# Optimization experiments

Measured on AMD Instinct MI355X. Metric: run time of the kernel, lower is better.

## Reference

```python
import jax, jax.numpy as jnp
import numpy as np
from jax import lax

LMBD = 0.1      # l1 penalty weight (init kwarg lmbd)
TOL = 1e-4      # convergence tolerance (init kwarg tol)
N_ITERS = 1000  # max ISTA iterations
DICT_SIZE = 1024
INPUT_DIM = 512
BATCH = 256


def setup_inputs() -> dict:
    key = jax.random.key(0)
    kx, kd = jax.random.split(key)
    # Dictionary parameter: randn rows normalized to unit l2 norm (as in _init_dict)
    D = jax.random.normal(kd, (DICT_SIZE, INPUT_DIM), dtype=jnp.float32)
    D = D / jnp.linalg.norm(D, axis=1, keepdims=True)
    x = jax.random.normal(kx, (BATCH, INPUT_DIM), dtype=jnp.float32)
    return {"x": x, "D": D}


def reference(x, D):
    # lr = 0.99 / max eigenvalue of Gram(D)  (as in _init_lr, done under no_grad)
    gram = D @ D.T  # [dict, dict]
    lr = 0.99 / jnp.max(jnp.linalg.eigvalsh(gram))
    thresh = lr * LMBD
    h0 = jnp.zeros((x.shape[0], D.shape[0]), dtype=x.dtype)  # [batch, dict]

    def cond(state):
        _, i, delta = state
        return (i < N_ITERS) & (delta >= TOL)

    def body(state):
        h, i, _ = state
        resid = x - h @ D          # [batch, input_dim]
        g = resid @ D.T            # [batch, dict]
        a = h + lr * g
        h_new = jnp.sign(a) * jnp.maximum(jnp.abs(a) - thresh, 0.0)  # soft-threshold
        delta = jnp.max(jnp.linalg.norm(h_new - h, axis=1))
        return (h_new, i + 1, delta)

    h, _, _ = lax.while_loop(cond, body, (h0, jnp.int32(0), jnp.float32(jnp.inf)))
    return h
```

## Files before the change

kernel.cpp:

```cpp
#include <hip/hip_runtime.h>
#include <math.h>

#define DICT 1024
#define IN_DIM 512
#define BATCH 256
#define LMBD_F 0.1f
#define TOL2 1e-8f
#define MAX_ITERS 1000
#define LM 64

#define OFF_G      0u
#define OFF_B      1048576u
#define OFF_HA     1310720u
#define OFF_W      1572864u
#define OFF_RDP    1573888u
#define OFF_FLG    1577984u
#define OFF_PM     1582080u
#define OFF_BF     1582592u
#define OFF_GBF    2106880u

typedef __attribute__((ext_vector_type(8))) short short8v;
typedef __attribute__((ext_vector_type(4))) float f32x4;
typedef __attribute__((ext_vector_type(4))) int i32x4;

#define MFMA16(a, b, c) __builtin_amdgcn_mfma_f32_16x16x32_bf16(a, b, c, 0, 0, 0)

__device__ __forceinline__ ushort f2bf(float v) {
    union { float f; unsigned u; } x; x.f = v;
    unsigned r = x.u + 0x7fffu + ((x.u >> 16) & 1u);
    return (ushort)(r >> 16);
}
__device__ __forceinline__ float bf2f(ushort b) {
    union { unsigned u; float f; } x; x.u = ((unsigned)b) << 16;
    return x.f;
}
__device__ __forceinline__ float softthr(float aa, float th) {
    float s = fabsf(aa) - th;
    return s > 0.f ? copysignf(s, aa) : 0.f;
}

__device__ __forceinline__ void vmdrain() { asm volatile("s_waitcnt vmcnt(0)" ::: "memory"); }
__device__ __forceinline__ unsigned ld_flag(const unsigned* p) {
    unsigned v;
    asm volatile("global_load_dword %0, %1, off sc1\ns_waitcnt vmcnt(0)" : "=v"(v) : "v"(p) : "memory");
    return v;
}
__device__ __forceinline__ void st_flag(unsigned* p, unsigned v) {
    asm volatile("global_store_dword %0, %1, off sc1" :: "v"(p), "v"(v) : "memory");
}
__device__ __forceinline__ float ld_f_sc(const float* p) {
    float v;
    asm volatile("global_load_dword %0, %1, off sc1\ns_waitcnt vmcnt(0)" : "=v"(v) : "v"(p) : "memory");
    return v;
}
__device__ __forceinline__ void st_f_sc(float* p, float v) {
    asm volatile("global_store_dword %0, %1, off sc1" :: "v"(p), "v"(v) : "memory");
}
__device__ __forceinline__ f32x4 ld_f4_sc(const float* p) {
    f32x4 v;
    asm volatile("global_load_dwordx4 %0, %1, off sc1\ns_waitcnt vmcnt(0)" : "=v"(v) : "v"(p) : "memory");
    return v;
}
__device__ __forceinline__ void st_u_sc(unsigned* p, unsigned v) {
    asm volatile("global_store_dword %0, %1, off sc1" :: "v"(p), "v"(v) : "memory");
}
__device__ __forceinline__ void ld_a16(i32x4* d, const void* p) {
    asm volatile("global_load_dwordx4 %0, %1, off sc1" : "=v"(*d) : "v"(p));
}
__device__ __forceinline__ void ld_u_nw(unsigned* d, const unsigned* p) {
    asm volatile("global_load_dword %0, %1, off sc1" : "=v"(*d) : "v"(p));
}
__device__ __forceinline__ void ld_f_nw(float* d, const float* p) {
    asm volatile("global_load_dword %0, %1, off sc1" : "=v"(*d) : "v"(p));
}

__global__ void k_init(float* ws) {
    int t = threadIdx.x;
    unsigned* flg = (unsigned*)(ws + OFF_FLG);
#pragma unroll
    for (int j = 0; j < 4; ++j) flg[t + 1024 * j] = 0u;
#pragma unroll
    for (int j = 0; j < 4; ++j) ws[OFF_RDP + t + 1024 * j] = 1e30f;
    if (t == 0) *(unsigned*)(ws + OFF_PM) = 0u;
}

__global__ void k_gemm_nt(float* __restrict__ C, const float* __restrict__ A,
                          const float* __restrict__ B, int M, int N, int K) {
    __shared__ float As[32][33];
    __shared__ float Bs[32][33];
    const int tid = threadIdx.x;
    const int m0 = blockIdx.y * 32, n0 = blockIdx.x * 32;
    const int lrw = tid >> 3;
    const int lc4 = (tid & 7) * 4;
    const int ty = tid >> 4, tx = tid & 15;
    float acc00 = 0, acc01 = 0, acc10 = 0, acc11 = 0;
    for (int k0 = 0; k0 < K; k0 += 32) {
        float4 av = *(const float4*)&A[(m0 + lrw) * K + k0 + lc4];
        float4 bv = *(const float4*)&B[(n0 + lrw) * K + k0 + lc4];
        __syncthreads();
        As[lrw][lc4 + 0] = av.x; As[lrw][lc4 + 1] = av.y;
        As[lrw][lc4 + 2] = av.z; As[lrw][lc4 + 3] = av.w;
        Bs[lrw][lc4 + 0] = bv.x; Bs[lrw][lc4 + 1] = bv.y;
        Bs[lrw][lc4 + 2] = bv.z; Bs[lrw][lc4 + 3] = bv.w;
        __syncthreads();
#pragma unroll
        for (int k = 0; k < 32; ++k) {
            float a0 = As[ty * 2][k], a1 = As[ty * 2 + 1][k];
            float b0 = Bs[tx * 2][k], b1 = Bs[tx * 2 + 1][k];
            acc00 += a0 * b0; acc01 += a0 * b1;
            acc10 += a1 * b0; acc11 += a1 * b1;
        }
    }
    C[(m0 + ty * 2) * N + n0 + tx * 2] = acc00;
    C[(m0 + ty * 2) * N + n0 + tx * 2 + 1] = acc01;
    C[(m0 + ty * 2 + 1) * N + n0 + tx * 2] = acc10;
    C[(m0 + ty * 2 + 1) * N + n0 + tx * 2 + 1] = acc11;
}

__global__ void k_conv_g(float* ws) {
    const int i = (blockIdx.x * 256 + threadIdx.x) * 4;
    const float* G = ws + OFF_G;
    ushort* Ghi = (ushort*)(ws + OFF_GBF);
    ushort* Glo = Ghi + 1048576u;
    float4 g = *(const float4*)&G[i];
    ushort h0 = f2bf(g.x), h1 = f2bf(g.y), h2 = f2bf(g.z), h3 = f2bf(g.w);
    *(ushort4*)&Ghi[i] = make_ushort4(h0, h1, h2, h3);
    ushort l0 = f2bf(g.x - bf2f(h0)), l1 = f2bf(g.y - bf2f(h1));
    ushort l2 = f2bf(g.z - bf2f(h2)), l3 = f2bf(g.w - bf2f(h3));
    *(ushort4*)&Glo[i] = make_ushort4(l0, l1, l2, l3);
}

__launch_bounds__(512, 2)
__global__ void k_persist(float* __restrict__ ws, float* __restrict__ dout) {
    const int tid = threadIdx.x;
    const int bid = blockIdx.x;
    const int w = tid >> 6, lane = tid & 63;
    unsigned* flg = (unsigned*)(ws + OFF_FLG);
    unsigned* podmask = (unsigned*)(ws + OFF_PM);
    float* Wg = ws + OFF_W;
    float* rdp = ws + OFF_RDP;
    const float* G = ws + OFF_G;

    __shared__ float Ps[8][16][64];
    __shared__ float Vl[1024], VPl[1024], Wl[1024];
    __shared__ float aArr[LM], bArr[LM];
    __shared__ float sred[8];
    __shared__ float scal2[2];
    __shared__ unsigned sres;
    __shared__ unsigned sbits[16];
    __shared__ unsigned sStick;

    unsigned gen = 0;

    const int bx = bid & 15;
    const int by = bid >> 4;
    const int R0 = by * 16, C0 = bx * 64;
    const int pod16 = by * 16;

    if (tid < 512) {
        Vl[tid] = 0.03125f; Vl[tid + 512] = 0.03125f;
        VPl[tid] = 0.f;     VPl[tid + 512] = 0.f;
    }
    __syncthreads();
    float bprev = 0.f;
#pragma unroll 1
    for (int j = 0; j < LM; ++j) {
        {
            const int row = tid >> 7, sub = tid & 127;
            const float* gr = G + (bid * 4 + row) * DICT;
            float s = 0.f;
#pragma unroll
            for (int jj = 0; jj < 8; ++jj) s += gr[sub + 128 * jj] * Vl[sub + 128 * jj];
#pragma unroll
            for (int off = 32; off; off >>= 1) s += __shfl_down(s, off);
            if (lane == 0) sred[w] = s;
            __syncthreads();
            if (tid < 4) st_f_sc(Wg + bid * 4 + tid, sred[2 * tid] + sred[2 * tid + 1]);
        }
        ++gen;
        vmdrain(); __syncthreads();
        if (tid == 0) st_flag(&flg[bid * 16], gen << 2);
        if (w == 0) {
            for (;;) {
                unsigned v0, v1, v2, v3;
                ld_u_nw(&v0, &flg[lane * 16]);
                ld_u_nw(&v1, &flg[(lane + 64) * 16]);
                ld_u_nw(&v2, &flg[(lane + 128) * 16]);
                ld_u_nw(&v3, &flg[(lane + 192) * 16]);
                vmdrain(); __builtin_amdgcn_sched_barrier(0);
                bool ok = ((v0 >> 2) >= gen) && ((v1 >> 2) >= gen) &&
                          ((v2 >> 2) >= gen) && ((v3 >> 2) >= gen);
                if (__ballot(ok) == ~0ull) break;
                __builtin_amdgcn_s_sleep(1);
            }
        }
        __syncthreads();
        if (tid < 256) { f32x4 w4 = ld_f4_sc(Wg + tid * 4); *(f32x4*)&Wl[tid * 4] = w4; }
        __syncthreads();
        float p = Vl[tid] * Wl[tid] + Vl[tid + 512] * Wl[tid + 512];
#pragma unroll
        for (int off = 32; off; off >>= 1) p += __shfl_down(p, off);
        if (lane == 0) sred[w] = p;
        __syncthreads();
        float alpha = sred[0] + sred[1] + sred[2] + sred[3] + sred[4] + sred[5] + sred[6] + sred[7];
        float u0 = Wl[tid] - alpha * Vl[tid] - bprev * VPl[tid];
        float u1 = Wl[tid + 512] - alpha * Vl[tid + 512] - bprev * VPl[tid + 512];
        float qq = u0 * u0 + u1 * u1;
        __syncthreads();
#pragma unroll
        for (int off = 32; off; off >>= 1) qq += __shfl_down(qq, off);
        if (lane == 0) sred[w] = qq;
        __syncthreads();
        float beta = sqrtf(sred[0] + sred[1] + sred[2] + sred[3] + sred[4] + sred[5] + sred[6] + sred[7]);
        float bsafe = (beta > 1e-20f) ? beta : 0.f;
        float inv = (beta > 1e-20f) ? 1.f / beta : 0.f;
        VPl[tid] = Vl[tid]; VPl[tid + 512] = Vl[tid + 512];
        Vl[tid] = u0 * inv; Vl[tid + 512] = u1 * inv;
        if (tid == 0) { aArr[j] = alpha; bArr[j] = bsafe; }
        bprev = bsafe;
        __syncthreads();
    }

    if (tid < 64) {
        double lo = 0.0, hi = 0.0;
        for (int i = 0; i < LM; ++i) {
            double bi  = fabs((double)bArr[i]);
            double bim = i ? fabs((double)bArr[i - 1]) : 0.0;
            double r = (double)aArr[i] + bi + bim;
            if (r > hi) hi = r;
        }
        for (int rnd = 0; rnd < 4; ++rnd) {
            double midt = lo + (hi - lo) * ((double)(tid + 1) / 65.0);
            int cntn = 0; double d = 1.0;
            for (int i = 0; i < LM; ++i) {
                double bm = i ? (double)bArr[i - 1] : 0.0;
                d = ((double)aArr[i] - midt) - (bm * bm) / d;
                if (d == 0.0) d = -1e-300;
                if (d < 0.0) cntn++;
            }
            unsigned long long m = __ballot(cntn >= LM);
            int first = (m == 0ull) ? 64 : (__ffsll((unsigned long long)m) - 1);
            double nlo = lo + (hi - lo) * ((double)first / 65.0);
            double nhi = (first == 64) ? hi : lo + (hi - lo) * ((double)(first + 1) / 65.0);
            lo = nlo; hi = nhi;
        }
        if (tid == 0) {
            float lam = (float)(0.5 * (lo + hi));
            float lrv = 0.99f / lam;
            scal2[0] = lrv;
            scal2[1] = lrv * LMBD_F;
        }
    }
    if (tid == 0) sStick = 0u;
    __syncthreads();
    const float lr = scal2[0], th = scal2[1];

    ushort* bfb = (ushort*)(ws + OFF_BF);
    const ushort* Ghi = (const ushort*)(ws + OFF_GBF);
    const float* bv_ = ws + OFF_B;
    float* hA = ws + OFF_HA;
    const int r16 = lane & 15, kk8 = (lane >> 4) * 8;
    const int er = tid >> 5;
    const int ec = (tid & 31) * 2;

    const ushort* pB = Ghi + (C0 + r16) * DICT + w * 128 + kk8;
    short8v bh[4][4], bl[4][4];
#pragma unroll
    for (int ks = 0; ks < 4; ++ks)
#pragma unroll
        for (int jj = 0; jj < 4; ++jj) {
            bh[ks][jj] = *(const short8v*)(pB + jj * 16 * DICT + ks * 32);
            bl[ks][jj] = *(const short8v*)(pB + 1048576u + jj * 16 * DICT + ks * 32);
        }

    unsigned sticky = 0, stPub = 0;
    const unsigned* fprod0 = &flg[(pod16 + 2 * w) * 16];
    const unsigned* fprod1 = &flg[(pod16 + 2 * w + 1) * 16];

#pragma unroll 1
    for (int it = 0; it < MAX_ITERS; ++it) {
        const float* h_in = (it & 1) ? hA : dout;
        float* h_out      = (it & 1) ? dout : hA;
        const ushort* hi_in = bfb + ((it & 1) ? 524288u : 0u);
        ushort* hi_out = bfb + ((it & 1) ? 0u : 524288u);

        if (lane < 2) {
            const unsigned* fp = lane ? fprod1 : fprod0;
            unsigned v; int spins = 0;
            for (;;) {
                v = ld_flag(fp);
                if ((v >> 2) >= gen) break;
                __builtin_amdgcn_s_sleep(1);
                if (++spins > (1 << 25)) break;
            }
            sbits[2 * w + lane] = ((v >> 2) == gen) ? ((v >> 1) & 1u) : (v & 1u);
        }
        const ushort* pA = hi_in + (R0 + r16) * DICT + w * 128 + kk8;
        i32x4 aHr[4], aLr[4];
#pragma unroll
        for (int ks = 0; ks < 4; ++ks) {
            ld_a16(&aHr[ks], (const void*)(pA + ks * 32));
            ld_a16(&aLr[ks], (const void*)(pA + 262144u + ks * 32));
        }
        asm volatile("s_waitcnt vmcnt(0)" ::: "memory");
        __builtin_amdgcn_sched_barrier(0);

        f32x4 aHH[4], aHL[4], aLH[4];
#pragma unroll
        for (int jj = 0; jj < 4; ++jj) {
            aHH[jj] = (f32x4){0.f, 0.f, 0.f, 0.f};
            aHL[jj] = (f32x4){0.f, 0.f, 0.f, 0.f};
            aLH[jj] = (f32x4){0.f, 0.f, 0.f, 0.f};
        }
#pragma unroll
        for (int ks = 0; ks < 4; ++ks) {
            short8v ah, al;
            __builtin_memcpy(&ah, &aHr[ks], 16);
            __builtin_memcpy(&al, &aLr[ks], 16);
#pragma unroll
            for (int jj = 0; jj < 4; ++jj) {
                aHH[jj] = MFMA16(ah, bh[ks][jj], aHH[jj]);
                aHL[jj] = MFMA16(ah, bl[ks][jj], aHL[jj]);
                aLH[jj] = MFMA16(al, bh[ks][jj], aLH[jj]);
            }
        }

        const int r0 = (lane >> 4) * 4;
#pragma unroll
        for (int jj = 0; jj < 4; ++jj) {
            f32x4 s = aHH[jj] + aHL[jj] + aLH[jj];
            const int col = 16 * jj + r16;
#pragma unroll
            for (int qq = 0; qq < 4; ++qq) Ps[w][r0 + qq][col] = s[qq];
        }
        __syncthreads();

        if (w == 0) {
            unsigned b = (lane < 16) ? sbits[lane] : 1u;
            unsigned long long allm = __ballot((b & 1u) != 0u);
            unsigned long long anym = __ballot((lane < 16) && ((b & 1u) != 0u));
            if (lane == 0) sres = ((allm == ~0ull) ? 2u : 0u) | ((anym != 0ull) ? 1u : 0u);
        }

        float s0 = 0.f, s1 = 0.f;
#pragma unroll
        for (int ww = 0; ww < 8; ++ww) { s0 += Ps[ww][er][ec]; s1 += Ps[ww][er][ec + 1]; }
        const int gi = (R0 + er) * DICT + C0 + ec;
        float2 bb = *(const float2*)&bv_[gi];
        float2 hh = *(const float2*)&h_in[gi];
        float n0 = softthr(hh.x + lr * (bb.x - s0), th);
        float n1 = softthr(hh.y + lr * (bb.y - s1), th);
        *(float2*)&h_out[gi] = make_float2(n0, n1);

        ushort q0 = f2bf(n0), q1 = f2bf(n1);
        st_u_sc((unsigned*)&hi_out[gi], ((unsigned)q1 << 16) | (unsigned)q0);
        ushort z0 = f2bf(n0 - bf2f(q0)), z1 = f2bf(n1 - bf2f(q1));
        st_u_sc((unsigned*)&hi_out[262144u + gi], ((unsigned)z1 << 16) | (unsigned)z0);

        float d0 = n0 - hh.x, d1 = n1 - hh.y;
        float ssq = d0 * d0 + d1 * d1;
#pragma unroll
        for (int off = 1; off < 32; off <<= 1) ssq += __shfl_xor(ssq, off);
        if ((tid & 31) == 0) st_f_sc(&rdp[bid * 16 + er], ssq);

        vmdrain();
        __syncthreads();
        const unsigned res = sres;
        sticky |= (res & 1u) | sStick;
        ++gen;
        if (res & 2u) {
            if ((it & 1) == 0) {
                const int g2 = (R0 + er) * DICT + C0 + ec;
                *(float2*)&dout[g2] = *(const float2*)&hA[g2];
            }
            return;
        }
        if (tid == 0) st_flag(&flg[bid * 16], (gen << 2) | (sticky << 1) | stPub);
        stPub = sticky;

        if (w == 1 && (it & 3) == 3 && bid == pod16 + ((it >> 2) & 15)) {
            float v0, v1, v2, v3;
            const float* rp = rdp + by * 256;
            ld_f_nw(&v0, rp + lane);
            ld_f_nw(&v1, rp + lane + 64);
            ld_f_nw(&v2, rp + lane + 128);
            ld_f_nw(&v3, rp + lane + 192);
            vmdrain(); __builtin_amdgcn_sched_barrier(0);
            float s = v0 + v1 + v2 + v3;
            s += __shfl_xor(s, 16);
            s += __shfl_xor(s, 32);
            float m = s;
            m = fmaxf(m, __shfl_xor(m, 1));
            m = fmaxf(m, __shfl_xor(m, 2));
            m = fmaxf(m, __shfl_xor(m, 4));
            m = fmaxf(m, __shfl_xor(m, 8));
            if (lane == 0) {
                if (m < TOL2)
                    __hip_atomic_fetch_or(podmask, 1u << by, __ATOMIC_RELAXED, __HIP_MEMORY_SCOPE_AGENT);
                unsigned pmv = ld_flag(podmask);
                if (pmv == 0xFFFFu) sStick = 1u;
            }
        }
    }
}

extern "C" void kernel_launch(void* const* d_in, const int* in_sizes, int n_in,
                              void* d_out, int out_size, void* d_ws, size_t ws_size,
                              hipStream_t stream) {
    const float* x = (const float*)d_in[0];
    const float* D = (const float*)d_in[1];
    float* out = (float*)d_out;
    float* ws = (float*)d_ws;

    (void)hipMemsetAsync(d_out, 0, (size_t)BATCH * DICT * sizeof(float), stream);
    (void)hipMemsetAsync((char*)(ws + OFF_BF), 0, 1048576, stream);
    k_init<<<dim3(1), dim3(1024), 0, stream>>>(ws);

    k_gemm_nt<<<dim3(32, 32), dim3(256), 0, stream>>>(ws + OFF_G, D, D, 1024, 1024, 512);
    k_conv_g<<<dim3(1024), dim3(256), 0, stream>>>(ws);
    k_gemm_nt<<<dim3(32, 8), dim3(256), 0, stream>>>(ws + OFF_B, x, D, 256, 1024, 512);

    void* args[] = { (void*)&ws, (void*)&out };
    (void)hipLaunchCooperativeKernel((const void*)k_persist, dim3(256), dim3(512), args, 0, stream);
}
```

Baseline: 4.585 ms.

## Keep fp32 h and b in registers, prefetch flags, cut residual-norm stores

Each thread now holds its fp32 h elements and its b values in registers across iterations, so the per-iteration global loads and stores of h and b go away. The output is written only once, at exit, which also removes the output memset. The neighbour flag is prefetched with a non-waiting load at the end of each iteration, and per-row squared deltas are stored only on the iterations when a convergence check reads them. This trims global memory traffic and latency on the critical path of every iteration. It relies on each thread owning a fixed element for the whole loop, and on the prefetched flag value being safe to reuse in the next spin.

```diff
diff --git a/kernel.cpp b/kernel.cpp
--- a/kernel.cpp
+++ b/kernel.cpp
@@ -258,7 +258,6 @@
     ushort* bfb = (ushort*)(ws + OFF_BF);
     const ushort* Ghi = (const ushort*)(ws + OFF_GBF);
     const float* bv_ = ws + OFF_B;
-    float* hA = ws + OFF_HA;
     const int r16 = lane & 15, kk8 = (lane >> 4) * 8;
     const int er = tid >> 5;
     const int ec = (tid & 31) * 2;
@@ -273,21 +272,26 @@
             bl[ks][jj] = *(const short8v*)(pB + 1048576u + jj * 16 * DICT + ks * 32);
         }
 
+    const int gi0 = (R0 + er) * DICT + C0 + ec;
+    const float2 breg = *(const float2*)&bv_[gi0];
+    float hc0 = 0.f, hc1 = 0.f;
+
     unsigned sticky = 0, stPub = 0;
     const unsigned* fprod0 = &flg[(pod16 + 2 * w) * 16];
     const unsigned* fprod1 = &flg[(pod16 + 2 * w + 1) * 16];
+    unsigned vpre = 0;
 
 #pragma unroll 1
     for (int it = 0; it < MAX_ITERS; ++it) {
-        const float* h_in = (it & 1) ? hA : dout;
-        float* h_out      = (it & 1) ? dout : hA;
         const ushort* hi_in = bfb + ((it & 1) ? 524288u : 0u);
         ushort* hi_out = bfb + ((it & 1) ? 0u : 524288u);
 
+        if (it > 0) vmdrain();
         if (lane < 2) {
             const unsigned* fp = lane ? fprod1 : fprod0;
-            unsigned v; int spins = 0;
-            for (;;) {
+            unsigned v = (it > 0) ? vpre : 0u;
+            int spins = 0;
+            while ((v >> 2) < gen) {
                 v = ld_flag(fp);
                 if ((v >> 2) >= gen) break;
                 __builtin_amdgcn_s_sleep(1);
@@ -345,23 +349,20 @@
         float s0 = 0.f, s1 = 0.f;
 #pragma unroll
         for (int ww = 0; ww < 8; ++ww) { s0 += Ps[ww][er][ec]; s1 += Ps[ww][er][ec + 1]; }
-        const int gi = (R0 + er) * DICT + C0 + ec;
-        float2 bb = *(const float2*)&bv_[gi];
-        float2 hh = *(const float2*)&h_in[gi];
-        float n0 = softthr(hh.x + lr * (bb.x - s0), th);
-        float n1 = softthr(hh.y + lr * (bb.y - s1), th);
-        *(float2*)&h_out[gi] = make_float2(n0, n1);
+        float n0 = softthr(hc0 + lr * (breg.x - s0), th);
+        float n1 = softthr(hc1 + lr * (breg.y - s1), th);
 
         ushort q0 = f2bf(n0), q1 = f2bf(n1);
-        st_u_sc((unsigned*)&hi_out[gi], ((unsigned)q1 << 16) | (unsigned)q0);
+        st_u_sc((unsigned*)&hi_out[gi0], ((unsigned)q1 << 16) | (unsigned)q0);
         ushort z0 = f2bf(n0 - bf2f(q0)), z1 = f2bf(n1 - bf2f(q1));
-        st_u_sc((unsigned*)&hi_out[262144u + gi], ((unsigned)z1 << 16) | (unsigned)z0);
-
-        float d0 = n0 - hh.x, d1 = n1 - hh.y;
+        st_u_sc((unsigned*)&hi_out[262144u + gi0], ((unsigned)z1 << 16) | (unsigned)z0);
+
+        float d0 = n0 - hc0, d1 = n1 - hc1;
+        hc0 = n0; hc1 = n1;
         float ssq = d0 * d0 + d1 * d1;
 #pragma unroll
         for (int off = 1; off < 32; off <<= 1) ssq += __shfl_xor(ssq, off);
-        if ((tid & 31) == 0) st_f_sc(&rdp[bid * 16 + er], ssq);
+        if ((it & 3) == 3 && (tid & 31) == 0) st_f_sc(&rdp[bid * 16 + er], ssq);
 
         vmdrain();
         __syncthreads();
@@ -369,10 +370,7 @@
         sticky |= (res & 1u) | sStick;
         ++gen;
         if (res & 2u) {
-            if ((it & 1) == 0) {
-                const int g2 = (R0 + er) * DICT + C0 + ec;
-                *(float2*)&dout[g2] = *(const float2*)&hA[g2];
-            }
+            *(float2*)&dout[gi0] = make_float2(hc0, hc1);
             return;
         }
         if (tid == 0) st_flag(&flg[bid * 16], (gen << 2) | (sticky << 1) | stPub);
@@ -401,7 +399,10 @@
                 if (pmv == 0xFFFFu) sStick = 1u;
             }
         }
+
+        if (lane < 2) ld_u_nw(&vpre, lane ? fprod1 : fprod0);
     }
+    *(float2*)&dout[gi0] = make_float2(hc0, hc1);
 }
 
 extern "C" void kernel_launch(void* const* d_in, const int* in_sizes, int n_in,
@@ -412,7 +413,6 @@
     float* out = (float*)d_out;
     float* ws = (float*)d_ws;
 
-    (void)hipMemsetAsync(d_out, 0, (size_t)BATCH * DICT * sizeof(float), stream);
     (void)hipMemsetAsync((char*)(ws + OFF_BF), 0, 1048576, stream);
     k_init<<<dim3(1), dim3(1024), 0, stream>>>(ws);
 
```

Result: slower. 4.751 ms (+3.6%).
